# Optimization experiments

Measured on AMD Instinct MI355X. Metric: run time of the kernel, lower is better.

Reference implementation:

```python
import jax, jax.numpy as jnp
import numpy as np

D = H = W = 128
C = 16
VOXEL_SIZE = 0.05  # origin = 0, grid spans [0, 6.4]^3 in world coords
N_POINTS = 2_000_000


def setup_inputs() -> dict:
    key = jax.random.key(0)
    k1, k2 = jax.random.split(key)
    # world-space query points uniformly inside the grid bounds
    points = jax.random.uniform(k1, (N_POINTS, 3), dtype=jnp.float32) * (D * VOXEL_SIZE)
    values = jax.random.normal(k2, (D, H, W, C), dtype=jnp.float32)
    return {"points": points, "values": values}


def reference(points, values):
    # world -> grid coords (origin = 0)
    gc = points / VOXEL_SIZE  # [N, 3]
    x, y, z = gc[:, 0], gc[:, 1], gc[:, 2]

    x0 = jnp.clip(jnp.floor(x).astype(jnp.int32), 0, D - 1)
    y0 = jnp.clip(jnp.floor(y).astype(jnp.int32), 0, H - 1)
    z0 = jnp.clip(jnp.floor(z).astype(jnp.int32), 0, W - 1)
    x1 = jnp.clip(x0 + 1, 0, D - 1)
    y1 = jnp.clip(y0 + 1, 0, H - 1)
    z1 = jnp.clip(z0 + 1, 0, W - 1)

    # fractional offsets (computed against the clipped floor index, as in source)
    xd = (x - x0.astype(x.dtype))[:, None]
    yd = (y - y0.astype(y.dtype))[:, None]
    zd = (z - z0.astype(z.dtype))[:, None]

    # flatten grid for efficient single-axis gather
    flat = values.reshape(D * H * W, C)

    def gather(xi, yi, zi):
        lin = (xi * H + yi) * W + zi  # [N]
        return jnp.take(flat, lin, axis=0)  # [N, C]

    c000 = gather(x0, y0, z0)
    c001 = gather(x0, y0, z1)
    c010 = gather(x0, y1, z0)
    c011 = gather(x0, y1, z1)
    c100 = gather(x1, y0, z0)
    c101 = gather(x1, y0, z1)
    c110 = gather(x1, y1, z0)
    c111 = gather(x1, y1, z1)

    c00 = c000 * (1 - xd) + c100 * xd
    c01 = c001 * (1 - xd) + c101 * xd
    c10 = c010 * (1 - xd) + c110 * xd
    c11 = c011 * (1 - xd) + c111 * xd
    c0 = c00 * (1 - yd) + c10 * yd
    c1 = c01 * (1 - yd) + c11 * yd
    return c0 * (1 - zd) + c1 * zd  # [N, C]
```

## Files before the change

### kernel.cpp

```cpp
#include <hip/hip_runtime.h>


#define DD 128
#define HH 128
#define WW 128

__device__ __forceinline__ float4 lerp4(float4 a, float4 b, float t) {
    return make_float4(fmaf(b.x - a.x, t, a.x),
                       fmaf(b.y - a.y, t, a.y),
                       fmaf(b.z - a.z, t, a.z),
                       fmaf(b.w - a.w, t, a.w));
}

__global__ __launch_bounds__(256) void trilerp_kernel(
    const float* __restrict__ points,
    const float4* __restrict__ values,
    float4* __restrict__ out,
    int n_points)
{
    int t = blockIdx.x * blockDim.x + threadIdx.x;
    int p = t >> 2;
    int c4 = t & 3;
    if (p >= n_points) return;

    float x = points[p * 3 + 0] * 20.0f;
    float y = points[p * 3 + 1] * 20.0f;
    float z = points[p * 3 + 2] * 20.0f;

    float fx = floorf(x), fy = floorf(y), fz = floorf(z);
    int x0 = min(max((int)fx, 0), DD - 1);
    int y0 = min(max((int)fy, 0), HH - 1);
    int z0 = min(max((int)fz, 0), WW - 1);
    int x1 = min(x0 + 1, DD - 1);
    int y1 = min(y0 + 1, HH - 1);
    int z1 = min(z0 + 1, WW - 1);

    float xd = x - (float)x0;
    float yd = y - (float)y0;
    float zd = z - (float)z0;

    #define VIDX(xi, yi, zi) (((((xi) << 7) + (yi)) << 7) + (zi)) * 4 + c4

    float4 c000 = values[VIDX(x0, y0, z0)];
    float4 c001 = values[VIDX(x0, y0, z1)];
    float4 c010 = values[VIDX(x0, y1, z0)];
    float4 c011 = values[VIDX(x0, y1, z1)];
    float4 c100 = values[VIDX(x1, y0, z0)];
    float4 c101 = values[VIDX(x1, y0, z1)];
    float4 c110 = values[VIDX(x1, y1, z0)];
    float4 c111 = values[VIDX(x1, y1, z1)];
    #undef VIDX

    float4 c00 = lerp4(c000, c100, xd);
    float4 c01 = lerp4(c001, c101, xd);
    float4 c10 = lerp4(c010, c110, xd);
    float4 c11 = lerp4(c011, c111, xd);

    float4 c0 = lerp4(c00, c10, yd);
    float4 c1 = lerp4(c01, c11, yd);

    out[t] = lerp4(c0, c1, zd);
}

extern "C" void kernel_launch(void* const* d_in, const int* in_sizes, int n_in,
                              void* d_out, int out_size, void* d_ws, size_t ws_size,
                              hipStream_t stream) {
    const float* points = (const float*)d_in[0];
    const float4* values = (const float4*)d_in[1];
    float4* out = (float4*)d_out;

    int n_points = in_sizes[0] / 3;
    int total_threads = n_points * 4;
    int blocks = (total_threads + 255) / 256;

    trilerp_kernel<<<blocks, 256, 0, stream>>>(points, values, out, n_points);
}
```

Baseline: 414.5 us.

## Bin points by spatial brick before interpolation to improve gather locality

Adds a scatter pass that buckets each point into one of 4096 8^3-voxel bricks using atomic cursors, writing compact records to workspace. A second kernel processes one brick per block, so the eight corner gathers hit a small, cache-resident region of the grid. Overflowing bins fall back to direct interpolation in the scatter pass. The cost is an extra memset, atomics, record traffic and scattered output writes, and the path only runs when enough workspace is available.

```diff
diff --git a/kernel.cpp b/kernel.cpp
--- a/kernel.cpp
+++ b/kernel.cpp
@@ -4,12 +4,107 @@
 #define DD 128
 #define HH 128
 #define WW 128
+#define NBX 16
+#define NB (NBX * NBX * NBX)
+#define CAP 640
+#define CUR_STRIDE 16
+
+typedef float fvec4 __attribute__((ext_vector_type(4)));
 
 __device__ __forceinline__ float4 lerp4(float4 a, float4 b, float t) {
     return make_float4(fmaf(b.x - a.x, t, a.x),
                        fmaf(b.y - a.y, t, a.y),
                        fmaf(b.z - a.z, t, a.z),
                        fmaf(b.w - a.w, t, a.w));
+}
+
+__device__ __forceinline__ int clampi(int v, int lo, int hi) {
+    return min(max(v, lo), hi);
+}
+
+__device__ __forceinline__ float4 trilerp_point(const float4* __restrict__ values,
+                                                float x, float y, float z, int c4) {
+    float fx = floorf(x), fy = floorf(y), fz = floorf(z);
+    int x0 = clampi((int)fx, 0, DD - 1);
+    int y0 = clampi((int)fy, 0, HH - 1);
+    int z0 = clampi((int)fz, 0, WW - 1);
+    int x1 = min(x0 + 1, DD - 1);
+    int y1 = min(y0 + 1, HH - 1);
+    int z1 = min(z0 + 1, WW - 1);
+
+    float xd = x - (float)x0;
+    float yd = y - (float)y0;
+    float zd = z - (float)z0;
+
+    #define VIDX(xi, yi, zi) ((((((xi) << 7) + (yi)) << 7) + (zi)) * 4 + c4)
+    float4 c000 = values[VIDX(x0, y0, z0)];
+    float4 c001 = values[VIDX(x0, y0, z1)];
+    float4 c010 = values[VIDX(x0, y1, z0)];
+    float4 c011 = values[VIDX(x0, y1, z1)];
+    float4 c100 = values[VIDX(x1, y0, z0)];
+    float4 c101 = values[VIDX(x1, y0, z1)];
+    float4 c110 = values[VIDX(x1, y1, z0)];
+    float4 c111 = values[VIDX(x1, y1, z1)];
+    #undef VIDX
+
+    float4 c00 = lerp4(c000, c100, xd);
+    float4 c01 = lerp4(c001, c101, xd);
+    float4 c10 = lerp4(c010, c110, xd);
+    float4 c11 = lerp4(c011, c111, xd);
+    float4 c0  = lerp4(c00, c10, yd);
+    float4 c1  = lerp4(c01, c11, yd);
+    return lerp4(c0, c1, zd);
+}
+
+__global__ __launch_bounds__(256) void scatter_kernel(
+    const float* __restrict__ points,
+    unsigned* __restrict__ cursors,
+    float4* __restrict__ recs,
+    const float4* __restrict__ values,
+    float4* __restrict__ out,
+    int n_points)
+{
+    int p = blockIdx.x * blockDim.x + threadIdx.x;
+    if (p >= n_points) return;
+
+    float x = points[p * 3 + 0] * 20.0f;
+    float y = points[p * 3 + 1] * 20.0f;
+    float z = points[p * 3 + 2] * 20.0f;
+
+    int bx = clampi((int)floorf(x), 0, DD - 1) >> 3;
+    int by = clampi((int)floorf(y), 0, HH - 1) >> 3;
+    int bz = clampi((int)floorf(z), 0, WW - 1) >> 3;
+    int b = (bx * NBX + by) * NBX + bz;
+
+    unsigned pos = atomicAdd(&cursors[b * CUR_STRIDE], 1u);
+    if (pos < CAP) {
+        float4 r = make_float4(x, y, z, __uint_as_float((unsigned)p));
+        recs[(unsigned)b * CAP + pos] = r;
+    } else {
+        #pragma unroll
+        for (int c = 0; c < 4; ++c)
+            out[p * 4 + c] = trilerp_point(values, x, y, z, c);
+    }
+}
+
+__global__ __launch_bounds__(256) void interp_kernel(
+    const float4* __restrict__ recs,
+    const unsigned* __restrict__ cursors,
+    const float4* __restrict__ values,
+    float4* __restrict__ out)
+{
+    int b = blockIdx.x;
+    unsigned cnt = cursors[b * CUR_STRIDE];
+    if (cnt > CAP) cnt = CAP;
+    unsigned base = (unsigned)b * CAP;
+    int c4 = threadIdx.x & 3;
+
+    for (unsigned j = threadIdx.x >> 2; j < cnt; j += 64) {
+        float4 r = recs[base + j];
+        float4 res = trilerp_point(values, r.x, r.y, r.z, c4);
+        unsigned idx = __float_as_uint(r.w);
+        __builtin_nontemporal_store(*(fvec4*)&res, (fvec4*)(out + ((size_t)idx * 4 + c4)));
+    }
 }
 
 __global__ __launch_bounds__(256) void trilerp_kernel(
@@ -26,40 +121,7 @@
     float x = points[p * 3 + 0] * 20.0f;
     float y = points[p * 3 + 1] * 20.0f;
     float z = points[p * 3 + 2] * 20.0f;
-
-    float fx = floorf(x), fy = floorf(y), fz = floorf(z);
-    int x0 = min(max((int)fx, 0), DD - 1);
-    int y0 = min(max((int)fy, 0), HH - 1);
-    int z0 = min(max((int)fz, 0), WW - 1);
-    int x1 = min(x0 + 1, DD - 1);
-    int y1 = min(y0 + 1, HH - 1);
-    int z1 = min(z0 + 1, WW - 1);
-
-    float xd = x - (float)x0;
-    float yd = y - (float)y0;
-    float zd = z - (float)z0;
-
-    #define VIDX(xi, yi, zi) (((((xi) << 7) + (yi)) << 7) + (zi)) * 4 + c4
-
-    float4 c000 = values[VIDX(x0, y0, z0)];
-    float4 c001 = values[VIDX(x0, y0, z1)];
-    float4 c010 = values[VIDX(x0, y1, z0)];
-    float4 c011 = values[VIDX(x0, y1, z1)];
-    float4 c100 = values[VIDX(x1, y0, z0)];
-    float4 c101 = values[VIDX(x1, y0, z1)];
-    float4 c110 = values[VIDX(x1, y1, z0)];
-    float4 c111 = values[VIDX(x1, y1, z1)];
-    #undef VIDX
-
-    float4 c00 = lerp4(c000, c100, xd);
-    float4 c01 = lerp4(c001, c101, xd);
-    float4 c10 = lerp4(c010, c110, xd);
-    float4 c11 = lerp4(c011, c111, xd);
-
-    float4 c0 = lerp4(c00, c10, yd);
-    float4 c1 = lerp4(c01, c11, yd);
-
-    out[t] = lerp4(c0, c1, zd);
+    out[t] = trilerp_point(values, x, y, z, c4);
 }
 
 extern "C" void kernel_launch(void* const* d_in, const int* in_sizes, int n_in,
@@ -70,8 +132,23 @@
     float4* out = (float4*)d_out;
 
     int n_points = in_sizes[0] / 3;
-    int total_threads = n_points * 4;
-    int blocks = (total_threads + 255) / 256;
 
-    trilerp_kernel<<<blocks, 256, 0, stream>>>(points, values, out, n_points);
+    const size_t cursors_bytes = (size_t)NB * CUR_STRIDE * sizeof(unsigned);
+    const size_t recs_bytes = (size_t)NB * CAP * sizeof(float4);
+    const size_t required = cursors_bytes + recs_bytes;
+
+    if (d_ws != nullptr && ws_size >= required) {
+        unsigned* cursors = (unsigned*)d_ws;
+        float4* recs = (float4*)((char*)d_ws + cursors_bytes);
+
+        hipMemsetAsync(cursors, 0, cursors_bytes, stream);
+
+        int blocks = (n_points + 255) / 256;
+        scatter_kernel<<<blocks, 256, 0, stream>>>(points, cursors, recs, values, out, n_points);
+        interp_kernel<<<NB, 256, 0, stream>>>(recs, cursors, values, out);
+    } else {
+        int total_threads = n_points * 4;
+        int blocks = (total_threads + 255) / 256;
+        trilerp_kernel<<<blocks, 256, 0, stream>>>(points, values, out, n_points);
+    }
 }
```

Measured after the change: 480.1 us. +15.8%, slower.

## Split each point across eight lanes and combine z-corners with cross-lane shuffle

Applied to the files above, without the earlier changes.

Each point is now handled by eight threads rather than four: four channel-quads times two z-corners. Each thread gathers four corners instead of eight, interpolates in x and y, then swaps partial results with a lane-xor shuffle so half the lanes finish the z interpolation and write the output. The aim is more memory-level parallelism and lower per-thread register pressure for the random gathers. In exchange it launches twice as many threads, reads the point coordinates twice as often, and leaves half the lanes idle during the store.

```diff
diff --git a/kernel.cpp b/kernel.cpp
--- a/kernel.cpp
+++ b/kernel.cpp
@@ -12,16 +12,18 @@
                        fmaf(b.w - a.w, t, a.w));
 }
 
-__global__ __launch_bounds__(256) void trilerp_kernel(
+__global__ __launch_bounds__(256) void trilerp_octet(
     const float* __restrict__ points,
     const float4* __restrict__ values,
     float4* __restrict__ out,
     int n_points)
 {
     int t = blockIdx.x * blockDim.x + threadIdx.x;
-    int p = t >> 2;
-    int c4 = t & 3;
+    int p = t >> 3;
     if (p >= n_points) return;
+    int e = t & 7;
+    int q = e & 3;
+    int s = e >> 2;
 
     float x = points[p * 3 + 0] * 20.0f;
     float y = points[p * 3 + 1] * 20.0f;
@@ -39,27 +41,29 @@
     float yd = y - (float)y0;
     float zd = z - (float)z0;
 
-    #define VIDX(xi, yi, zi) (((((xi) << 7) + (yi)) << 7) + (zi)) * 4 + c4
+    int zs = s ? z1 : z0;
 
-    float4 c000 = values[VIDX(x0, y0, z0)];
-    float4 c001 = values[VIDX(x0, y0, z1)];
-    float4 c010 = values[VIDX(x0, y1, z0)];
-    float4 c011 = values[VIDX(x0, y1, z1)];
-    float4 c100 = values[VIDX(x1, y0, z0)];
-    float4 c101 = values[VIDX(x1, y0, z1)];
-    float4 c110 = values[VIDX(x1, y1, z0)];
-    float4 c111 = values[VIDX(x1, y1, z1)];
+    #define VIDX(xi, yi) ((((((xi) << 7) + (yi)) << 7) + zs) * 4 + q)
+    float4 A = values[VIDX(x0, y0)];
+    float4 B = values[VIDX(x0, y1)];
+    float4 C = values[VIDX(x1, y0)];
+    float4 D = values[VIDX(x1, y1)];
     #undef VIDX
 
-    float4 c00 = lerp4(c000, c100, xd);
-    float4 c01 = lerp4(c001, c101, xd);
-    float4 c10 = lerp4(c010, c110, xd);
-    float4 c11 = lerp4(c011, c111, xd);
+    float4 u = lerp4(A, C, xd);
+    float4 v = lerp4(B, D, xd);
+    float4 w = lerp4(u, v, yd);
 
-    float4 c0 = lerp4(c00, c10, yd);
-    float4 c1 = lerp4(c01, c11, yd);
+    float4 o4;
+    o4.x = __shfl_xor(w.x, 4);
+    o4.y = __shfl_xor(w.y, 4);
+    o4.z = __shfl_xor(w.z, 4);
+    o4.w = __shfl_xor(w.w, 4);
 
-    out[t] = lerp4(c0, c1, zd);
+    if (s == 0) {
+        float4 res = lerp4(w, o4, zd);
+        out[(size_t)p * 4 + q] = res;
+    }
 }
 
 extern "C" void kernel_launch(void* const* d_in, const int* in_sizes, int n_in,
@@ -70,8 +74,8 @@
     float4* out = (float4*)d_out;
 
     int n_points = in_sizes[0] / 3;
-    int total_threads = n_points * 4;
-    int blocks = (total_threads + 255) / 256;
+    long long total_threads = (long long)n_points * 8;
+    int blocks = (int)((total_threads + 255) / 256);
 
-    trilerp_kernel<<<blocks, 256, 0, stream>>>(points, values, out, n_points);
+    trilerp_octet<<<blocks, 256, 0, stream>>>(points, values, out, n_points);
 }
```

Result: no change. 408.2 us (-1.5%).
